# Kernel optimization log

Hardware: AMD Instinct MI355X
Metric: run time of the kernel (lower is better)

Reference implementation:

```python
import jax, jax.numpy as jnp
import numpy as np

EPS = 0.2        # noise magnitude (init eps)
N_LAYERS = 3     # n_layers
LAYER_CL = 1     # layer_cl
U, I, D = 100000, 50000, 64
E = 2000000
N = U + I


def setup_inputs() -> dict:
    key = jax.random.key(0)
    k1, k2, k3, k4, k5, k6 = jax.random.split(key, 6)
    user_emb = jax.random.normal(k1, (U, D), dtype=jnp.float32) * 0.1
    item_emb = jax.random.normal(k2, (I, D), dtype=jnp.float32) * 0.1
    edge_rows = jax.random.randint(k3, (E,), 0, N, dtype=jnp.int32)
    edge_cols = jax.random.randint(k4, (E,), 0, N, dtype=jnp.int32)
    # symmetric-normalized Laplacian values are small positive floats
    edge_vals = jax.random.uniform(k5, (E,), dtype=jnp.float32) * 0.1
    noise = jax.random.uniform(k6, (N_LAYERS, N, D), dtype=jnp.float32)
    return {"user_emb": user_emb, "item_emb": item_emb,
            "edge_rows": edge_rows, "edge_cols": edge_cols,
            "edge_vals": edge_vals, "noise": noise}


def _spmm(vals, rows, cols, x, n):
    # sparse (COO) @ dense: gather source rows, scale, scatter-add to dest rows
    return jax.ops.segment_sum(vals[:, None] * x[cols], rows, num_segments=n)


def reference(user_emb, item_emb, edge_rows, edge_cols, edge_vals, noise):
    n = user_emb.shape[0] + item_emb.shape[0]
    ego = jnp.concatenate([user_emb, item_emb], axis=0)      # [N, D]
    acc = jnp.zeros_like(ego)
    cl = ego
    for k in range(N_LAYERS):
        ego = _spmm(edge_vals, edge_rows, edge_cols, ego, n)
        # F.normalize(rand, dim=-1) (eps=1e-12), then sign-aligned perturbation
        nk = noise[k]
        nk = nk / jnp.maximum(jnp.linalg.norm(nk, axis=-1, keepdims=True), 1e-12)
        ego = ego + jnp.sign(ego) * nk * EPS
        acc = acc + ego
        if k == LAYER_CL - 1:
            cl = ego
    final = acc / N_LAYERS                                   # mean over layer stack
    # rows [:N] = mean-pooled embeddings (split user/item at U);
    # rows [N:] = contrastive-layer embeddings (all_embeddings_cl)
    return jnp.concatenate([final, cl], axis=0)              # [2N, D]
```

## Files before the change

### kernel.cpp

```cpp
#include <hip/hip_runtime.h>

#define UCNT 100000
#define NN   150000
#define DD   64
#define EE   2000000
#define EPSV 0.2f

#define BROWS   64
#define NBUCK   2344
#define NCHUNK  128
#define CEDGE   15628
#define CAP     1536

#define MTOT    (NBUCK * NCHUNK)
#define SC_BLK  256
#define SC_EL   2048
#define SC_NB   ((MTOT + SC_EL - 1) / SC_EL)

__global__ __launch_bounds__(512) void passA_hist(const int* __restrict__ rows,
                                                  int* __restrict__ countA) {
    __shared__ int h[NBUCK];
    for (int b = threadIdx.x; b < NBUCK; b += 512) h[b] = 0;
    __syncthreads();
    int c = blockIdx.x;
    int e0 = c * CEDGE;
    int e1 = e0 + CEDGE; if (e1 > EE) e1 = EE;
    const int4* rows4 = (const int4*)rows;
    for (int i4 = (e0 >> 2) + threadIdx.x; i4 < (e1 >> 2); i4 += 512) {
        int4 r4 = rows4[i4];
        atomicAdd(&h[r4.x >> 6], 1);
        atomicAdd(&h[r4.y >> 6], 1);
        atomicAdd(&h[r4.z >> 6], 1);
        atomicAdd(&h[r4.w >> 6], 1);
    }
    __syncthreads();
    for (int b = threadIdx.x; b < NBUCK; b += 512)
        countA[b * NCHUNK + c] = h[b];
}

__global__ void scanA2(const int* __restrict__ in, int* __restrict__ outx,
                       int* __restrict__ bsum) {
    int b = blockIdx.x, t = threadIdx.x;
    int i0 = b * SC_EL + t * 8;
    int v[8]; int s = 0;
    #pragma unroll
    for (int u = 0; u < 8; ++u) {
        int i = i0 + u;
        v[u] = (i < MTOT) ? in[i] : 0;
        s += v[u];
    }
    __shared__ int lds[SC_BLK];
    lds[t] = s; __syncthreads();
    for (int off = 1; off < SC_BLK; off <<= 1) {
        int add = (t >= off) ? lds[t - off] : 0;
        __syncthreads(); lds[t] += add; __syncthreads();
    }
    int excl = lds[t] - s;
    #pragma unroll
    for (int u = 0; u < 8; ++u) {
        int i = i0 + u;
        if (i < MTOT) outx[i] = excl;
        excl += v[u];
    }
    if (t == SC_BLK - 1) bsum[b] = lds[t];
}

__global__ void scanB2(int* __restrict__ bsum, int nb) {
    int t = threadIdx.x;
    int v = (t < nb) ? bsum[t] : 0;
    __shared__ int lds[SC_BLK];
    lds[t] = v; __syncthreads();
    for (int off = 1; off < SC_BLK; off <<= 1) {
        int add = (t >= off) ? lds[t - off] : 0;
        __syncthreads(); lds[t] += add; __syncthreads();
    }
    if (t < nb) bsum[t] = lds[t] - v;
}

__global__ void scanC2(int* __restrict__ outx, const int* __restrict__ bsum) {
    int b = blockIdx.x, t = threadIdx.x;
    int add = bsum[b];
    int i0 = b * SC_EL + t * 8;
    #pragma unroll
    for (int u = 0; u < 8; ++u) {
        int i = i0 + u;
        if (i < MTOT) outx[i] += add;
    }
}

__global__ __launch_bounds__(512) void passC_scatter(const int* __restrict__ rows,
                                                     const int* __restrict__ cols,
                                                     const float* __restrict__ vals,
                                                     const int* __restrict__ seg,
                                                     int4* __restrict__ rec) {
    __shared__ int cur[NBUCK];
    int c = blockIdx.x;
    for (int b = threadIdx.x; b < NBUCK; b += 512) cur[b] = seg[b * NCHUNK + c];
    __syncthreads();
    int e0 = c * CEDGE;
    int e1 = e0 + CEDGE; if (e1 > EE) e1 = EE;
    const int4*   rows4 = (const int4*)rows;
    const int4*   cols4 = (const int4*)cols;
    const float4* vals4 = (const float4*)vals;
    for (int i4 = (e0 >> 2) + threadIdx.x; i4 < (e1 >> 2); i4 += 512) {
        int4   r4 = rows4[i4];
        int4   c4 = cols4[i4];
        float4 v4 = vals4[i4];
        int e = i4 << 2;
        int pos;
        pos = atomicAdd(&cur[r4.x >> 6], 1);
        rec[pos] = make_int4(r4.x, c4.x, __float_as_int(v4.x), e + 0);
        pos = atomicAdd(&cur[r4.y >> 6], 1);
        rec[pos] = make_int4(r4.y, c4.y, __float_as_int(v4.y), e + 1);
        pos = atomicAdd(&cur[r4.z >> 6], 1);
        rec[pos] = make_int4(r4.z, c4.z, __float_as_int(v4.z), e + 2);
        pos = atomicAdd(&cur[r4.w >> 6], 1);
        rec[pos] = make_int4(r4.w, c4.w, __float_as_int(v4.w), e + 3);
    }
}

__global__ __launch_bounds__(256) void passD_final(const int4* __restrict__ rec,
                                                   const int* __restrict__ seg,
                                                   int* __restrict__ counts,
                                                   int* __restrict__ basep,
                                                   int2* __restrict__ cpair) {
    int b = blockIdx.x;
    int rb = b * BROWS;
    int seg0 = seg[b * NCHUNK];
    int seg1 = (b + 1 < NBUCK) ? seg[(b + 1) * NCHUNK] : EE;
    int tot = seg1 - seg0;
    __shared__ int hist[BROWS], baseL[BROWS], cur[BROWS];
    __shared__ unsigned eidL[CAP];
    __shared__ int2 pairL[CAP];
    int t = threadIdx.x;
    if (t < BROWS) hist[t] = 0;
    __syncthreads();
    if (tot <= CAP) {
        for (int i = t; i < tot; i += 256)
            atomicAdd(&hist[rec[seg0 + i].x & (BROWS - 1)], 1);
        __syncthreads();
        if (t < BROWS) {
            int v = hist[t];
            int inc = v;
            for (int off = 1; off < BROWS; off <<= 1) {
                int o = __shfl_up(inc, off, 64);
                if (t >= off) inc += o;
            }
            baseL[t] = inc - v;
            cur[t]   = inc - v;
            int r = rb + t;
            if (r < NN) { counts[r] = v; basep[r] = seg0 + inc - v; }
        }
        __syncthreads();
        for (int i = t; i < tot; i += 256) {
            int4 q = rec[seg0 + i];
            int rl = q.x & (BROWS - 1);
            int d = atomicAdd(&cur[rl], 1);
            eidL[d]  = (unsigned)q.w;
            pairL[d] = make_int2(q.y, q.z);
        }
        __syncthreads();
        int w = t >> 6, lane = t & 63;
        int r0w = w * 16;
        for (int g = 0; g < 16; g += 4) {
            int rl = r0w + g + (lane >> 4);
            int n  = hist[rl];
            int l16 = lane & 15;
            int sl = baseL[rl];
            bool use = (n <= 16) && (l16 < n);
            unsigned key = 0xFFFFFFFFu; int pc = 0, pv = 0;
            if (use) {
                key = eidL[sl + l16];
                int2 p = pairL[sl + l16];
                pc = p.x; pv = p.y;
            }
            #pragma unroll
            for (int k = 2; k <= 16; k <<= 1) {
                #pragma unroll
                for (int j = k >> 1; j > 0; j >>= 1) {
                    unsigned ok = __shfl_xor(key, j, 64);
                    int oc = __shfl_xor(pc, j, 64), ov = __shfl_xor(pv, j, 64);
                    bool up = ((l16 & k) == 0), lower = ((l16 & j) == 0);
                    bool take = (lower == up) ? (ok < key) : (ok > key);
                    if (take) { key = ok; pc = oc; pv = ov; }
                }
            }
            if (use) cpair[seg0 + sl + l16] = make_int2(pc, pv);
        }
        {
            int myn = (lane < 16) ? hist[r0w + lane] : 0;
            unsigned long long big = __ballot(lane < 16 && myn > 16);
            while (big) {
                int ia = __ffsll((long long)big) - 1; big &= big - 1;
                int ib = -1;
                if (big) { ib = __ffsll((long long)big) - 1; big &= big - 1; }
                int na = hist[r0w + ia];
                int nb2 = (ib >= 0) ? hist[r0w + ib] : 0;
                if (na <= 32 && nb2 <= 32) {
                    int rid = (lane < 32) ? ia : ((ib >= 0) ? ib : ia);
                    int rl  = r0w + rid;
                    int n   = (lane < 32) ? na : nb2;
                    int l32 = lane & 31;
                    int sl  = baseL[rl];
                    bool act = (lane < 32) || (ib >= 0);
                    bool use = act && (l32 < n);
                    unsigned key = 0xFFFFFFFFu; int pc = 0, pv = 0;
                    if (use) {
                        key = eidL[sl + l32];
                        int2 p = pairL[sl + l32];
                        pc = p.x; pv = p.y;
                    }
                    #pragma unroll
                    for (int k = 2; k <= 32; k <<= 1) {
                        #pragma unroll
                        for (int j = k >> 1; j > 0; j >>= 1) {
                            unsigned ok = __shfl_xor(key, j, 64);
                            int oc = __shfl_xor(pc, j, 64), ov = __shfl_xor(pv, j, 64);
                            bool up = ((l32 & k) == 0), lower = ((l32 & j) == 0);
                            bool take = (lower == up) ? (ok < key) : (ok > key);
                            if (take) { key = ok; pc = oc; pv = ov; }
                        }
                    }
                    if (use) cpair[seg0 + sl + l32] = make_int2(pc, pv);
                } else {
                    for (int ps = 0; ps < 2; ++ps) {
                        int rid = (ps == 0) ? ia : ib;
                        if (rid < 0) continue;
                        int rl = r0w + rid;
                        int n = hist[rl];
                        int sl = baseL[rl];
                        if (n <= 16) continue;
                        if (n <= 64) {
                            unsigned key = 0xFFFFFFFFu; int pc = 0, pv = 0;
                            if (lane < n) {
                                key = eidL[sl + lane];
                                int2 p = pairL[sl + lane];
                                pc = p.x; pv = p.y;
                            }
                            #pragma unroll
                            for (int k = 2; k <= 64; k <<= 1) {
                                #pragma unroll
                                for (int j = k >> 1; j > 0; j >>= 1) {
                                    unsigned ok = __shfl_xor(key, j, 64);
                                    int oc = __shfl_xor(pc, j, 64), ov = __shfl_xor(pv, j, 64);
                                    bool up = ((lane & k) == 0), lower = ((lane & j) == 0);
                                    bool take = (lower == up) ? (ok < key) : (ok > key);
                                    if (take) { key = ok; pc = oc; pv = ov; }
                                }
                            }
                            if (lane < n) cpair[seg0 + sl + lane] = make_int2(pc, pv);
                        } else if (lane == 0) {
                            for (int i = 1; i < n; ++i) {
                                unsigned kk = eidL[sl + i]; int2 pp = pairL[sl + i];
                                int j = i - 1;
                                while (j >= 0 && eidL[sl + j] > kk) {
                                    eidL[sl + j + 1]  = eidL[sl + j];
                                    pairL[sl + j + 1] = pairL[sl + j];
                                    --j;
                                }
                                eidL[sl + j + 1] = kk; pairL[sl + j + 1] = pp;
                            }
                            for (int i = 0; i < n; ++i)
                                cpair[seg0 + sl + i] = pairL[sl + i];
                        }
                    }
                }
            }
        }
    } else if (t == 0) {
        int off = seg0;
        for (int r = rb; r < rb + BROWS && r < NN; ++r) {
            int cnt = 0;
            for (int i = seg0; i < seg1; ++i) if (rec[i].x == r) cnt++;
            counts[r] = cnt; basep[r] = off;
            unsigned last = 0;
            for (int m = 0; m < cnt; ++m) {
                unsigned best = 0xFFFFFFFFu; int bc = 0, bv = 0;
                for (int i = seg0; i < seg1; ++i) {
                    int4 q = rec[i];
                    if (q.x == r) {
                        unsigned ee = (unsigned)q.w;
                        if (ee >= last && ee < best) { best = ee; bc = q.y; bv = q.z; }
                    }
                }
                cpair[off + m] = make_int2(bc, bv);
                last = best + 1;
            }
            off += cnt;
        }
    }
}

__device__ __forceinline__ float sgnf(float v) {
    return (v > 0.0f) ? 1.0f : ((v < 0.0f) ? -1.0f : 0.0f);
}

__global__ __launch_bounds__(256) void
spmm_fused(const int* __restrict__ base, const int* __restrict__ counts,
           const int2* __restrict__ cpair,
           const float* __restrict__ xu, const float* __restrict__ xi,
           int usplit,
           const float* __restrict__ noise_k,
           float* __restrict__ xout,
           const float* __restrict__ cl_in,
           const float* __restrict__ xa_in,
           float* __restrict__ outp,
           int k) {
    int tid = blockIdx.x * 256 + threadIdx.x;
    int row = tid >> 4;
    if (row >= NN) return;
    int lane = threadIdx.x & 63;
    int q  = lane & 15;
    int gb = lane & 48;

    int s = base[row];
    int n = counts[row];

    size_t ro = (size_t)row * DD + q * 4;
    float4 nv = *(const float4*)(noise_k + ro);
    float4 clv = make_float4(0.f, 0.f, 0.f, 0.f);
    float4 xav = make_float4(0.f, 0.f, 0.f, 0.f);
    if (k == 2) {
        clv = *(const float4*)(cl_in + ro);
        xav = *(const float4*)(xa_in + ro);
    }

    float4 acc = make_float4(0.f, 0.f, 0.f, 0.f);
    for (int chunk = 0; chunk < n; chunk += 16) {
        int rem = n - chunk;
        int m = (rem < 16) ? rem : 16;
        int2 p = make_int2(0, 0);
        if (q < rem) p = cpair[s + chunk + q];

        float  vv[16];
        float4 xv[16];
        #pragma unroll
        for (int i = 0; i < 16; ++i) {
            int   c = __shfl(p.x, gb + i, 64);
            vv[i]   = __int_as_float(__shfl(p.y, gb + i, 64));
            if (i < m) {
                const float* xr = (c < usplit) ? (xu + (size_t)c * DD)
                                               : (xi + (size_t)(c - usplit) * DD);
                xv[i] = ((const float4*)xr)[q];
            }
        }
        #pragma unroll
        for (int i = 0; i < 16; ++i) {
            if (i < m) {
                acc.x += vv[i] * xv[i].x;
                acc.y += vv[i] * xv[i].y;
                acc.z += vv[i] * xv[i].z;
                acc.w += vv[i] * xv[i].w;
            }
        }
    }

    float ss = nv.x * nv.x + nv.y * nv.y + nv.z * nv.z + nv.w * nv.w;
    ss += __shfl_xor(ss, 1, 64);
    ss += __shfl_xor(ss, 2, 64);
    ss += __shfl_xor(ss, 4, 64);
    ss += __shfl_xor(ss, 8, 64);
    float scale = EPSV / fmaxf(sqrtf(ss), 1e-12f);

    float4 ego;
    ego.x = acc.x + sgnf(acc.x) * nv.x * scale;
    ego.y = acc.y + sgnf(acc.y) * nv.y * scale;
    ego.z = acc.z + sgnf(acc.z) * nv.z * scale;
    ego.w = acc.w + sgnf(acc.w) * nv.w * scale;

    if (k == 2) {
        const float inv3 = 1.0f / 3.0f;
        float4 o;
        o.x = (clv.x + xav.x + ego.x) * inv3;
        o.y = (clv.y + xav.y + ego.y) * inv3;
        o.z = (clv.z + xav.z + ego.z) * inv3;
        o.w = (clv.w + xav.w + ego.w) * inv3;
        *(float4*)(outp + ro) = o;
    } else {
        *(float4*)(xout + ro) = ego;
    }
}

extern "C" void kernel_launch(void* const* d_in, const int* in_sizes, int n_in,
                              void* d_out, int out_size, void* d_ws, size_t ws_size,
                              hipStream_t stream) {
    const float* ue    = (const float*)d_in[0];
    const float* ie    = (const float*)d_in[1];
    const int*   erow  = (const int*)  d_in[2];
    const int*   ecol  = (const int*)  d_in[3];
    const float* evals = (const float*)d_in[4];
    const float* noise = (const float*)d_in[5];
    float* out = (float*)d_out;

    char* w = (char*)d_ws;
    float* x_a    = (float*)w;
    int4*  rec    = (int4*)w;                     w += (size_t)NN * DD * sizeof(float);
    int2*  cpair  = (int2*)w;                     w += (size_t)EE * sizeof(int2);
    int*   countA = (int*)w;                      w += (size_t)MTOT * sizeof(int);
    int*   segp   = (int*)w;                      w += (size_t)MTOT * sizeof(int);
    int*   bsum   = (int*)w;                      w += 256 * sizeof(int);
    int*   counts = (int*)w;                      w += (size_t)NN * sizeof(int);
    int*   basep  = (int*)w;                      w += (size_t)NN * sizeof(int);

    passA_hist<<<NCHUNK, 512, 0, stream>>>(erow, countA);
    scanA2<<<SC_NB, SC_BLK, 0, stream>>>(countA, segp, bsum);
    scanB2<<<1, SC_BLK, 0, stream>>>(bsum, SC_NB);
    scanC2<<<SC_NB, SC_BLK, 0, stream>>>(segp, bsum);
    passC_scatter<<<NCHUNK, 512, 0, stream>>>(erow, ecol, evals, segp, rec);
    passD_final<<<NBUCK, 256, 0, stream>>>(rec, segp, counts, basep, cpair);

    float* cl = out + (size_t)NN * DD;
    int grd = (NN + 15) / 16;
    const int IMAX = 0x7FFFFFFF;

    spmm_fused<<<grd, 256, 0, stream>>>(basep, counts, cpair,
                                        ue, ie, UCNT,
                                        noise + (size_t)0 * NN * DD,
                                        cl, nullptr, nullptr, nullptr, 0);
    spmm_fused<<<grd, 256, 0, stream>>>(basep, counts, cpair,
                                        cl, nullptr, IMAX,
                                        noise + (size_t)1 * NN * DD,
                                        x_a, nullptr, nullptr, nullptr, 1);
    spmm_fused<<<grd, 256, 0, stream>>>(basep, counts, cpair,
                                        x_a, nullptr, IMAX,
                                        noise + (size_t)2 * NN * DD,
                                        nullptr, cl, x_a, out, 2);
}
```

Baseline: 360.1 us.

## Split scatter records into compact cpair and packed aux keys; double chunk count

The bucket-scatter pass now writes the 8-byte (col,val) pair straight into its final cpair array, plus a 4-byte aux word that packs the local row (top 6 bits) with the edge id. The old pass wrote a 16-byte int4 record. This cuts scatter write traffic and lets passD read less data. The edge-chunk count is doubled to 256 for more parallelism in the histogram and scatter passes, and the scan block size is doubled to match. The overflow fallback becomes an in-place insertion sort on global memory. Packing assumes edge ids fit in 26 bits, and the larger chunk count doubles the size of the count and scan arrays.

After: 369.5 us. 2.6% more time.

```diff
diff --git a/kernel.cpp b/kernel.cpp
--- a/kernel.cpp
+++ b/kernel.cpp
@@ -8,14 +8,15 @@
 
 #define BROWS   64
 #define NBUCK   2344
-#define NCHUNK  128
-#define CEDGE   15628
+#define NCHUNK  256
+#define CEDGE   7816
 #define CAP     1536
 
 #define MTOT    (NBUCK * NCHUNK)
-#define SC_BLK  256
-#define SC_EL   2048
+#define SC_BLK  512
+#define SC_EL   4096
 #define SC_NB   ((MTOT + SC_EL - 1) / SC_EL)
+
 
 __global__ __launch_bounds__(512) void passA_hist(const int* __restrict__ rows,
                                                   int* __restrict__ countA) {
@@ -38,8 +39,9 @@
         countA[b * NCHUNK + c] = h[b];
 }
 
-__global__ void scanA2(const int* __restrict__ in, int* __restrict__ outx,
-                       int* __restrict__ bsum) {
+__global__ __launch_bounds__(SC_BLK) void scanA2(const int* __restrict__ in,
+                                                 int* __restrict__ outx,
+                                                 int* __restrict__ bsum) {
     int b = blockIdx.x, t = threadIdx.x;
     int i0 = b * SC_EL + t * 8;
     int v[8]; int s = 0;
@@ -68,16 +70,17 @@
 __global__ void scanB2(int* __restrict__ bsum, int nb) {
     int t = threadIdx.x;
     int v = (t < nb) ? bsum[t] : 0;
-    __shared__ int lds[SC_BLK];
+    __shared__ int lds[256];
     lds[t] = v; __syncthreads();
-    for (int off = 1; off < SC_BLK; off <<= 1) {
+    for (int off = 1; off < 256; off <<= 1) {
         int add = (t >= off) ? lds[t - off] : 0;
         __syncthreads(); lds[t] += add; __syncthreads();
     }
     if (t < nb) bsum[t] = lds[t] - v;
 }
 
-__global__ void scanC2(int* __restrict__ outx, const int* __restrict__ bsum) {
+__global__ __launch_bounds__(SC_BLK) void scanC2(int* __restrict__ outx,
+                                                 const int* __restrict__ bsum) {
     int b = blockIdx.x, t = threadIdx.x;
     int add = bsum[b];
     int i0 = b * SC_EL + t * 8;
@@ -92,7 +95,8 @@
                                                      const int* __restrict__ cols,
                                                      const float* __restrict__ vals,
                                                      const int* __restrict__ seg,
-                                                     int4* __restrict__ rec) {
+                                                     int2* __restrict__ cpair,
+                                                     unsigned* __restrict__ aux) {
     __shared__ int cur[NBUCK];
     int c = blockIdx.x;
     for (int b = threadIdx.x; b < NBUCK; b += 512) cur[b] = seg[b * NCHUNK + c];
@@ -109,21 +113,25 @@
         int e = i4 << 2;
         int pos;
         pos = atomicAdd(&cur[r4.x >> 6], 1);
-        rec[pos] = make_int4(r4.x, c4.x, __float_as_int(v4.x), e + 0);
+        cpair[pos] = make_int2(c4.x, __float_as_int(v4.x));
+        aux[pos] = ((unsigned)(r4.x & 63) << 26) | (unsigned)(e + 0);
         pos = atomicAdd(&cur[r4.y >> 6], 1);
-        rec[pos] = make_int4(r4.y, c4.y, __float_as_int(v4.y), e + 1);
+        cpair[pos] = make_int2(c4.y, __float_as_int(v4.y));
+        aux[pos] = ((unsigned)(r4.y & 63) << 26) | (unsigned)(e + 1);
         pos = atomicAdd(&cur[r4.z >> 6], 1);
-        rec[pos] = make_int4(r4.z, c4.z, __float_as_int(v4.z), e + 2);
+        cpair[pos] = make_int2(c4.z, __float_as_int(v4.z));
+        aux[pos] = ((unsigned)(r4.z & 63) << 26) | (unsigned)(e + 2);
         pos = atomicAdd(&cur[r4.w >> 6], 1);
-        rec[pos] = make_int4(r4.w, c4.w, __float_as_int(v4.w), e + 3);
-    }
-}
-
-__global__ __launch_bounds__(256) void passD_final(const int4* __restrict__ rec,
+        cpair[pos] = make_int2(c4.w, __float_as_int(v4.w));
+        aux[pos] = ((unsigned)(r4.w & 63) << 26) | (unsigned)(e + 3);
+    }
+}
+
+__global__ __launch_bounds__(256) void passD_final(unsigned* __restrict__ auxg,
                                                    const int* __restrict__ seg,
                                                    int* __restrict__ counts,
                                                    int* __restrict__ basep,
-                                                   int2* __restrict__ cpair) {
+                                                   int2* __restrict__ cpairg) {
     int b = blockIdx.x;
     int rb = b * BROWS;
     int seg0 = seg[b * NCHUNK];
@@ -137,7 +145,7 @@
     __syncthreads();
     if (tot <= CAP) {
         for (int i = t; i < tot; i += 256)
-            atomicAdd(&hist[rec[seg0 + i].x & (BROWS - 1)], 1);
+            atomicAdd(&hist[auxg[seg0 + i] >> 26], 1);
         __syncthreads();
         if (t < BROWS) {
             int v = hist[t];
@@ -153,11 +161,12 @@
         }
         __syncthreads();
         for (int i = t; i < tot; i += 256) {
-            int4 q = rec[seg0 + i];
-            int rl = q.x & (BROWS - 1);
+            unsigned a = auxg[seg0 + i];
+            int2 p = cpairg[seg0 + i];
+            int rl = (int)(a >> 26);
             int d = atomicAdd(&cur[rl], 1);
-            eidL[d]  = (unsigned)q.w;
-            pairL[d] = make_int2(q.y, q.z);
+            eidL[d]  = a;
+            pairL[d] = p;
         }
         __syncthreads();
         int w = t >> 6, lane = t & 63;
@@ -185,7 +194,7 @@
                     if (take) { key = ok; pc = oc; pv = ov; }
                 }
             }
-            if (use) cpair[seg0 + sl + l16] = make_int2(pc, pv);
+            if (use) cpairg[seg0 + sl + l16] = make_int2(pc, pv);
         }
         {
             int myn = (lane < 16) ? hist[r0w + lane] : 0;
@@ -221,7 +230,7 @@
                             if (take) { key = ok; pc = oc; pv = ov; }
                         }
                     }
-                    if (use) cpair[seg0 + sl + l32] = make_int2(pc, pv);
+                    if (use) cpairg[seg0 + sl + l32] = make_int2(pc, pv);
                 } else {
                     for (int ps = 0; ps < 2; ++ps) {
                         int rid = (ps == 0) ? ia : ib;
@@ -248,7 +257,7 @@
                                     if (take) { key = ok; pc = oc; pv = ov; }
                                 }
                             }
-                            if (lane < n) cpair[seg0 + sl + lane] = make_int2(pc, pv);
+                            if (lane < n) cpairg[seg0 + sl + lane] = make_int2(pc, pv);
                         } else if (lane == 0) {
                             for (int i = 1; i < n; ++i) {
                                 unsigned kk = eidL[sl + i]; int2 pp = pairL[sl + i];
@@ -261,32 +270,31 @@
                                 eidL[sl + j + 1] = kk; pairL[sl + j + 1] = pp;
                             }
                             for (int i = 0; i < n; ++i)
-                                cpair[seg0 + sl + i] = pairL[sl + i];
+                                cpairg[seg0 + sl + i] = pairL[sl + i];
                         }
                     }
                 }
             }
         }
     } else if (t == 0) {
-        int off = seg0;
-        for (int r = rb; r < rb + BROWS && r < NN; ++r) {
-            int cnt = 0;
-            for (int i = seg0; i < seg1; ++i) if (rec[i].x == r) cnt++;
-            counts[r] = cnt; basep[r] = off;
-            unsigned last = 0;
-            for (int m = 0; m < cnt; ++m) {
-                unsigned best = 0xFFFFFFFFu; int bc = 0, bv = 0;
-                for (int i = seg0; i < seg1; ++i) {
-                    int4 q = rec[i];
-                    if (q.x == r) {
-                        unsigned ee = (unsigned)q.w;
-                        if (ee >= last && ee < best) { best = ee; bc = q.y; bv = q.z; }
-                    }
-                }
-                cpair[off + m] = make_int2(bc, bv);
-                last = best + 1;
-            }
-            off += cnt;
+        for (int i = 1; i < tot; ++i) {
+            unsigned kk = auxg[seg0 + i]; int2 pp = cpairg[seg0 + i];
+            int j = i - 1;
+            while (j >= 0 && auxg[seg0 + j] > kk) {
+                auxg[seg0 + j + 1]  = auxg[seg0 + j];
+                cpairg[seg0 + j + 1] = cpairg[seg0 + j];
+                --j;
+            }
+            auxg[seg0 + j + 1] = kk; cpairg[seg0 + j + 1] = pp;
+        }
+        int idx = 0;
+        for (int rl = 0; rl < BROWS; ++rl) {
+            int r = rb + rl;
+            if (r >= NN) break;
+            int start = idx;
+            while (idx < tot && (int)(auxg[seg0 + idx] >> 26) == rl) ++idx;
+            counts[r] = idx - start;
+            basep[r]  = seg0 + start;
         }
     }
 }
@@ -393,21 +401,21 @@
     float* out = (float*)d_out;
 
     char* w = (char*)d_ws;
-    float* x_a    = (float*)w;
-    int4*  rec    = (int4*)w;                     w += (size_t)NN * DD * sizeof(float);
-    int2*  cpair  = (int2*)w;                     w += (size_t)EE * sizeof(int2);
-    int*   countA = (int*)w;                      w += (size_t)MTOT * sizeof(int);
-    int*   segp   = (int*)w;                      w += (size_t)MTOT * sizeof(int);
-    int*   bsum   = (int*)w;                      w += 256 * sizeof(int);
-    int*   counts = (int*)w;                      w += (size_t)NN * sizeof(int);
-    int*   basep  = (int*)w;                      w += (size_t)NN * sizeof(int);
+    float*    x_a    = (float*)w;
+    unsigned* aux    = (unsigned*)w;              w += (size_t)NN * DD * sizeof(float);
+    int2*     cpair  = (int2*)w;                  w += (size_t)EE * sizeof(int2);
+    int*      countA = (int*)w;                   w += (size_t)MTOT * sizeof(int);
+    int*      segp   = (int*)w;                   w += (size_t)MTOT * sizeof(int);
+    int*      bsum   = (int*)w;                   w += 256 * sizeof(int);
+    int*      counts = (int*)w;                   w += (size_t)NN * sizeof(int);
+    int*      basep  = (int*)w;                   w += (size_t)NN * sizeof(int);
 
     passA_hist<<<NCHUNK, 512, 0, stream>>>(erow, countA);
     scanA2<<<SC_NB, SC_BLK, 0, stream>>>(countA, segp, bsum);
-    scanB2<<<1, SC_BLK, 0, stream>>>(bsum, SC_NB);
+    scanB2<<<1, 256, 0, stream>>>(bsum, SC_NB);
     scanC2<<<SC_NB, SC_BLK, 0, stream>>>(segp, bsum);
-    passC_scatter<<<NCHUNK, 512, 0, stream>>>(erow, ecol, evals, segp, rec);
-    passD_final<<<NBUCK, 256, 0, stream>>>(rec, segp, counts, basep, cpair);
+    passC_scatter<<<NCHUNK, 512, 0, stream>>>(erow, ecol, evals, segp, cpair, aux);
+    passD_final<<<NBUCK, 256, 0, stream>>>(aux, segp, counts, basep, cpair);
 
     float* cl = out + (size_t)NN * DD;
     int grd = (NN + 15) / 16;
```
